# Performance work log

Measured on AMD Instinct MI355X. Metric: run time of the kernel, lower is better.

Reference implementation:

```python
import jax, jax.numpy as jnp
import numpy as np

DIM = 128
HEADS = 8
HEAD_DIM = DIM // HEADS
PE_DIM = 48
TEMP = 10000.0
WIN = 2
NUM_VALUES = WIN * WIN
SCALE = HEAD_DIM ** -0.5
TWO_PI = 2.0 * np.pi
EPS = 1e-6


def _interleave_sincos(p):
    # p [..., nf] -> interleaved sin(even)/cos(odd), matching torch stack+flatten
    s = jnp.sin(p[..., 0::2])
    c = jnp.cos(p[..., 1::2])
    return jnp.stack((s, c), axis=-1).reshape(p.shape)


def _dim_t(num_pos_feats):
    i = np.arange(num_pos_feats)
    return jnp.asarray(TEMP ** (2.0 * (i // 2) / num_pos_feats), dtype=jnp.float32)


def window_position_bias():
    nf = PE_DIM // 2
    ye = jnp.arange(WIN, dtype=jnp.float32)  # cumsum(ones)-1 along h
    xe = jnp.arange(WIN, dtype=jnp.float32)
    ye = ye / (ye[-1] + EPS) * TWO_PI
    xe = xe / (xe[-1] + EPS) * TWO_PI
    dt = _dim_t(nf)
    pos_y = ye[:, None, None] / dt
    pos_x = xe[None, :, None] / dt
    pos_y = jnp.broadcast_to(pos_y, (WIN, WIN, nf))
    pos_x = jnp.broadcast_to(pos_x, (WIN, WIN, nf))
    pe = jnp.concatenate((_interleave_sincos(pos_y), _interleave_sincos(pos_x)), axis=-1)
    return pe.reshape(NUM_VALUES, PE_DIM)


def points_position_encoding(points):
    # points [n, hw, 2] fractional offsets -> [n, hw, PE_DIM]
    nf = PE_DIM // 2
    ye = points[..., 0] / (WIN + EPS) * TWO_PI
    xe = points[..., 1] / (WIN + EPS) * TWO_PI
    dt = _dim_t(nf)
    pos_y = _interleave_sincos(ye[..., None] / dt)
    pos_x = _interleave_sincos(xe[..., None] / dt)
    return jnp.concatenate((pos_y, pos_x), axis=-1)


def setup_inputs() -> dict:
    key = jax.random.key(0)
    ks = jax.random.split(key, 12)
    n, c, h, w = 2, 48, 192, 192
    y = jax.random.normal(ks[0], (n, c, h, w), jnp.float32)
    x = jax.random.normal(ks[1], (n, c, h, w), jnp.float32)
    conv_w = jax.random.normal(ks[2], (1, 2 * PE_DIM, 3, 3), jnp.float32) * 0.05
    conv_b = jnp.zeros((1,), jnp.float32)
    q_w = jax.random.normal(ks[3], (PE_DIM, DIM), jnp.float32) * (PE_DIM ** -0.5)
    q_b = jnp.zeros((DIM,), jnp.float32)
    k_w = jax.random.normal(ks[4], (PE_DIM, DIM), jnp.float32) * (PE_DIM ** -0.5)
    k_b = jnp.zeros((DIM,), jnp.float32)
    v_w = jax.random.normal(ks[5], (PE_DIM, DIM), jnp.float32) * (PE_DIM ** -0.5)
    v_b = jnp.zeros((DIM,), jnp.float32)
    return {"y": y, "x": x, "conv_w": conv_w, "conv_b": conv_b,
            "q_w": q_w, "q_b": q_b, "k_w": k_w, "k_b": k_b, "v_w": v_w, "v_b": v_b}


def reference(y, x, conv_w, conv_b, q_w, q_b, k_w, k_b, v_w, v_b):
    n, c, h, w = x.shape
    hw = h * w
    # per-pixel horizontal offset from both feature maps
    off = jax.lax.conv_general_dilated(
        jnp.concatenate([y, x], axis=1), conv_w, (1, 1), ((1, 1), (1, 1)),
        dimension_numbers=("NCHW", "OIHW", "NCHW")) + conv_b[None, :, None, None]
    off = jnp.transpose(off, (0, 2, 3, 1)) * (2.0 / w)  # [n,h,w,1]

    gh, gw = jnp.meshgrid(jnp.arange(h, dtype=x.dtype), jnp.arange(w, dtype=x.dtype), indexing="ij")
    # flow.flip(-1) puts the offset on the w coordinate only
    grid_wrp = jnp.stack(
        (jnp.broadcast_to(gh, (n, h, w)),
         gw[None] + off[..., 0]), axis=-1)                      # [n,h,w,2]
    flr = jnp.floor(grid_wrp)
    frac = (grid_wrp - flr).reshape(n, hw, 2)
    flr = flr.reshape(n, hw, 2)

    widx = jnp.array([[0, 0], [0, 1], [1, 0], [1, 1]], dtype=x.dtype)  # window_idx_offset
    g4 = (flr[:, :, None, :] + widx).reshape(n, hw * NUM_VALUES, 2)

    idx0 = jnp.clip(g4[..., 0], 0, h - 1).astype(jnp.int32)
    idx1 = jnp.clip(g4[..., 1], 0, w - 1).astype(jnp.int32)
    lin = idx1 + w * idx0                                      # [n, hw*4]
    wrp = jnp.take_along_axis(y.reshape(n, c, hw), lin[:, None, :], axis=2)  # [n,c,hw*4]
    wrp = jnp.transpose(wrp, (0, 2, 1))                        # [n, hw*4, c]

    # pe_dim // c == 1 tiling; add window position bias per pixel
    pb = window_position_bias()                                # [4, PE_DIM]
    wrp = (wrp.reshape(n, hw, NUM_VALUES, PE_DIM) + pb).reshape(n, hw * NUM_VALUES, PE_DIM)

    x_flat = jnp.transpose(x.reshape(n, c, hw), (0, 2, 1))     # [n, hw, c]
    x_in = x_flat + points_position_encoding(frac)

    nhw = n * hw
    q = (x_in @ q_w + q_b).reshape(nhw, HEADS, HEAD_DIM)
    k = (wrp @ k_w + k_b).reshape(nhw, NUM_VALUES, HEADS, HEAD_DIM)
    v = (wrp @ v_w + v_b).reshape(nhw, NUM_VALUES, HEADS, HEAD_DIM)

    attn = jnp.einsum("phd,pkhd->phk", q * SCALE, k)           # [nhw, heads, 4]
    attn = jax.nn.softmax(attn, axis=-1)
    out = jnp.einsum("phk,pkhd->phd", attn, v).reshape(nhw, DIM)
    return jnp.transpose(out.reshape(n, h, w, DIM), (0, 3, 1, 2))
```

## Files before the change

kernel.cpp:

```cpp
#include <hip/hip_runtime.h>
#include <hip/hip_bf16.h>

#define HW_ 36864
#define W_ 192
#define H_ 192
#define NPIX_ 73728
#define TWO_PI_F 6.283185307179586f

typedef __attribute__((ext_vector_type(8))) short bfrag;
typedef __attribute__((ext_vector_type(4))) float f4;

__device__ __constant__ float DT_G[12] = {
    1.0f, 2.154434690031884f, 4.641588833612779f, 10.0f,
    21.54434690031884f, 46.41588833612779f, 100.0f, 215.4434690031884f,
    464.1588833612779f, 1000.0f, 2154.434690031884f, 4641.588833612779f};

__device__ __forceinline__ unsigned short f2bf(float f) {
    __hip_bfloat16 h = __float2bfloat16(f);
    unsigned short u;
    __builtin_memcpy(&u, &h, 2);
    return u;
}

__device__ __forceinline__ int a_idx(int tile, int m, int k) {
    return tile * 1024 + ((k >> 5) << 9) + (m << 3) + (((k >> 3) & 3) << 7) + (k & 7);
}

__global__ void prep_wfrag(const float* __restrict__ qw, const float* __restrict__ kw,
                           const float* __restrict__ vw, unsigned short* __restrict__ wsb) {
    int idx = blockIdx.x * 256 + threadIdx.x;
    if (idx >= 24576) return;
    int j = idx & 7;
    int lane = (idx >> 3) & 63;
    int ks = (idx >> 9) & 1;
    int h = (idx >> 10) & 7;
    int mat = idx >> 13;
    const float* w = (mat == 0) ? qw : (mat == 1) ? kw : vw;
    int k = ks * 32 + ((lane >> 4) << 3) + j;
    int n = (h << 4) + (lane & 15);
    float f = (k < 48) ? w[k * 128 + n] : 0.0f;
    wsb[idx] = f2bf(f);
}

__global__ __launch_bounds__(256, 4) void conv_kernel(
    const float* __restrict__ y, const float* __restrict__ x,
    const float* __restrict__ cw, const float* __restrict__ cb,
    float* __restrict__ offs_g) {
    __shared__ float part[8][64];
    int tid = threadIdx.x;
    int bid = blockIdx.x;
    int b = (bid & 7) * 144 + (bid >> 3);
    int pix0 = b * 64;
    int n = pix0 / HW_;
    int rem = pix0 - n * HW_;
    int row0 = rem / W_;
    int col0 = rem - row0 * W_;
    int lane = tid & 63, w = tid >> 6;
    int col = col0 + lane;

    float m_lf = (col > 0) ? 1.f : 0.f, m_rt = (col < W_ - 1) ? 1.f : 0.f;
    float m_up = (row0 > 0) ? 1.f : 0.f, m_dn = (row0 < H_ - 1) ? 1.f : 0.f;
    int c_lf = col - (col > 0 ? 1 : 0);
    int c_rt = col + (col < W_ - 1 ? 1 : 0);
    int r_up = row0 - (row0 > 0 ? 1 : 0);
    int r_dn = row0 + (row0 < H_ - 1 ? 1 : 0);
    float k0 = m_up * m_lf, k1 = m_up, k2 = m_up * m_rt;
    float k3 = m_lf, k5 = m_rt;
    float k6 = m_dn * m_lf, k7 = m_dn, k8 = m_dn * m_rt;

    float accA = 0.f, accB = 0.f;
#pragma unroll
    for (int g = 0; g < 4; ++g) {
        float buf[54];
#pragma unroll
        for (int cc = 0; cc < 6; ++cc) {
            int ic = w * 24 + g * 6 + cc;
            const float* src = (ic < 48) ? y : x;
            int c = (ic < 48) ? ic : ic - 48;
            const float* b0 = src + (size_t)(n * 48 + c) * HW_;
            const float* pu = b0 + (size_t)r_up * W_;
            const float* pm = b0 + (size_t)row0 * W_;
            const float* pd = b0 + (size_t)r_dn * W_;
            buf[cc * 9 + 0] = pu[c_lf];
            buf[cc * 9 + 1] = pu[col];
            buf[cc * 9 + 2] = pu[c_rt];
            buf[cc * 9 + 3] = pm[c_lf];
            buf[cc * 9 + 4] = pm[col];
            buf[cc * 9 + 5] = pm[c_rt];
            buf[cc * 9 + 6] = pd[c_lf];
            buf[cc * 9 + 7] = pd[col];
            buf[cc * 9 + 8] = pd[c_rt];
        }
        float& acc = (g < 2) ? accA : accB;
#pragma unroll
        for (int cc = 0; cc < 6; ++cc) {
            int ic = w * 24 + g * 6 + cc;
            const float* wp = cw + ic * 9;
            acc += buf[cc * 9 + 0] * (wp[0] * k0);
            acc += buf[cc * 9 + 1] * (wp[1] * k1);
            acc += buf[cc * 9 + 2] * (wp[2] * k2);
            acc += buf[cc * 9 + 3] * (wp[3] * k3);
            acc += buf[cc * 9 + 4] * wp[4];
            acc += buf[cc * 9 + 5] * (wp[5] * k5);
            acc += buf[cc * 9 + 6] * (wp[6] * k6);
            acc += buf[cc * 9 + 7] * (wp[7] * k7);
            acc += buf[cc * 9 + 8] * (wp[8] * k8);
        }
    }
    part[2 * w][lane] = accA;
    part[2 * w + 1][lane] = accB;
    __syncthreads();
    if (tid < 64) {
        float a = part[0][tid];
#pragma unroll
        for (int s = 1; s < 8; ++s) a += part[s][tid];
        offs_g[pix0 + tid] = (a + cb[0]) * (2.0f / (float)W_);
    }
}

struct __align__(16) Smem {
    unsigned short A[10 * 1024];
    float outt[128 * 33];
    float pbl[192];
    float offs[32];
};

__global__ __launch_bounds__(512, 6) void fused_kernel(
    const float* __restrict__ y, const float* __restrict__ x,
    const float* __restrict__ qb, const float* __restrict__ kb,
    const float* __restrict__ vb, const unsigned short* __restrict__ wsb,
    const float* __restrict__ offs_g, float* __restrict__ out) {
    __shared__ Smem sm;
    int tid = threadIdx.x;
    int bid = blockIdx.x;
    int b = (bid & 7) * 288 + (bid >> 3);
    int pix0 = b * 32;
    int n = pix0 / HW_;
    int rem0 = pix0 - n * HW_;
    int row0 = rem0 / W_;
    int col0 = rem0 - row0 * W_;

    float xv[3];
    {
        int p = tid & 31, c0 = tid >> 5;
        const float* xb = x + (size_t)(n * 48) * HW_ + rem0 + p;
#pragma unroll
        for (int k2 = 0; k2 < 3; ++k2) xv[k2] = xb[(size_t)(c0 + 16 * k2) * HW_];
    }

    if (tid < 32) sm.offs[tid] = offs_g[pix0 + tid];
    if (tid < 192) {
        int v = tid / 48, c = tid - (tid / 48) * 48;
        int iy = v >> 1, ix = v & 1;
        int cc = (c < 24) ? c : c - 24;
        int sel = (c < 24) ? iy : ix;
        float e = sel ? (TWO_PI_F / (1.0f + 1e-6f)) : 0.0f;
        int j = cc >> 1;
        float arg = e / DT_G[j];
        sm.pbl[v * 48 + c] = (cc & 1) ? __cosf(arg) : __sinf(arg);
    }
    for (int i = tid; i < 1280; i += 512) {
        int t = i >> 7;
        ((unsigned int*)sm.A)[t * 512 + 384 + (i & 127)] = 0u;
    }
    __syncthreads();

    {
        int p = tid & 31, c0 = tid >> 5;
        float o = sm.offs[p];
        float gx = (float)(col0 + p) + o;
        float fr = gx - floorf(gx);
        float t1 = fr / (2.0f + 1e-6f);
#pragma unroll
        for (int k2 = 0; k2 < 3; ++k2) {
            int c = c0 + 16 * k2;
            float pe;
            if (c < 24) {
                pe = (c & 1) ? 1.0f : 0.0f;
            } else {
                int cc = c - 24;
                float arg = (t1 * TWO_PI_F) / DT_G[cc >> 1];
                pe = (cc & 1) ? __cosf(arg) : __sinf(arg);
            }
            sm.A[a_idx(p >> 4, p & 15, c)] = f2bf(xv[k2] + pe);
        }
    }
    {
        int r = tid & 127, cH = tid >> 7;
        int p = r >> 2, v = r & 3;
        float o = sm.offs[p];
        float gx = (float)(col0 + p) + o;
        float fx = floorf(gx);
        int dy = v >> 1, dx = v & 1;
        int rr = (int)fminf(fmaxf((float)(row0 + dy), 0.0f), 191.0f);
        int ccx = (int)fminf(fmaxf(fx + (float)dx, 0.0f), 191.0f);
        const float* yb = y + (size_t)(n * 48 + cH) * HW_ + rr * W_ + ccx;
        float yv[12];
#pragma unroll
        for (int k2 = 0; k2 < 12; ++k2) yv[k2] = yb[(size_t)(4 * k2) * HW_];
        int t = 2 + (r >> 4), m = r & 15;
#pragma unroll
        for (int k2 = 0; k2 < 12; ++k2) {
            int c = cH + 4 * k2;
            sm.A[a_idx(t, m, c)] = f2bf(yv[k2] + sm.pbl[v * 48 + c]);
        }
    }
    __syncthreads();

    int lane = tid & 63, h = tid >> 6;
    int lq = lane & 15, lg = lane >> 4;
    float qbv = qb[(h << 4) + lq];
    float kbv = kb[(h << 4) + lq];
    float vbv = vb[(h << 4) + lq];

    const int hb = (h << 1) * 64 + lane;
    bfrag qB0 = *(const bfrag*)&wsb[(0 * 1024 + hb) * 8];
    bfrag qB1 = *(const bfrag*)&wsb[(0 * 1024 + hb + 64) * 8];
    bfrag kB0 = *(const bfrag*)&wsb[(1 * 1024 + hb) * 8];
    bfrag kB1 = *(const bfrag*)&wsb[(1 * 1024 + hb + 64) * 8];
    bfrag vB0 = *(const bfrag*)&wsb[(2 * 1024 + hb) * 8];
    bfrag vB1 = *(const bfrag*)&wsb[(2 * 1024 + hb + 64) * 8];

    f4 qacc[2];
#pragma unroll
    for (int t = 0; t < 2; ++t) {
        bfrag a0 = *(const bfrag*)&sm.A[t * 1024 + lane * 8];
        bfrag a1 = *(const bfrag*)&sm.A[t * 1024 + 512 + lane * 8];
        f4 a = {qbv, qbv, qbv, qbv};
        a = __builtin_amdgcn_mfma_f32_16x16x32_bf16(a0, qB0, a, 0, 0, 0);
        a = __builtin_amdgcn_mfma_f32_16x16x32_bf16(a1, qB1, a, 0, 0, 0);
        qacc[t] = a;
    }

#pragma unroll
    for (int m = 0; m < 8; ++m) {
        bfrag a0 = *(const bfrag*)&sm.A[(2 + m) * 1024 + lane * 8];
        bfrag a1 = *(const bfrag*)&sm.A[(2 + m) * 1024 + 512 + lane * 8];
        f4 ka = {kbv, kbv, kbv, kbv};
        ka = __builtin_amdgcn_mfma_f32_16x16x32_bf16(a0, kB0, ka, 0, 0, 0);
        ka = __builtin_amdgcn_mfma_f32_16x16x32_bf16(a1, kB1, ka, 0, 0, 0);
        f4 va = {vbv, vbv, vbv, vbv};
        va = __builtin_amdgcn_mfma_f32_16x16x32_bf16(a0, vB0, va, 0, 0, 0);
        va = __builtin_amdgcn_mfma_f32_16x16x32_bf16(a1, vB1, va, 0, 0, 0);

        int src = ((m & 3) << 4) | lq;
        f4 qa = qacc[m >> 2];
        float t0 = __shfl(qa.x, src), t1 = __shfl(qa.y, src);
        float t2 = __shfl(qa.z, src), t3 = __shfl(qa.w, src);
        float qv = (lg == 0) ? t0 : (lg == 1) ? t1 : (lg == 2) ? t2 : t3;
        qv *= 0.25f;

        float s0 = qv * ka.x, s1 = qv * ka.y, s2 = qv * ka.z, s3 = qv * ka.w;
#pragma unroll
        for (int msk = 1; msk < 16; msk <<= 1) {
            s0 += __shfl_xor(s0, msk);
            s1 += __shfl_xor(s1, msk);
            s2 += __shfl_xor(s2, msk);
            s3 += __shfl_xor(s3, msk);
        }
        float mx = fmaxf(fmaxf(s0, s1), fmaxf(s2, s3));
        float e0 = __expf(s0 - mx), e1 = __expf(s1 - mx);
        float e2 = __expf(s2 - mx), e3 = __expf(s3 - mx);
        float rden = 1.0f / (e0 + e1 + e2 + e3);
        float o = (e0 * va.x + e1 * va.y + e2 * va.z + e3 * va.w) * rden;
        sm.outt[((h << 4) + lq) * 33 + (m << 2) + lg] = o;
    }
    __syncthreads();

    {
        int ch = tid >> 2, q4 = tid & 3;
        const float* sp = &sm.outt[ch * 33 + q4 * 8];
        float4* dst = (float4*)(out + (size_t)(n * 128 + ch) * HW_ + rem0 + q4 * 8);
        dst[0] = make_float4(sp[0], sp[1], sp[2], sp[3]);
        dst[1] = make_float4(sp[4], sp[5], sp[6], sp[7]);
    }
}

extern "C" void kernel_launch(void* const* d_in, const int* in_sizes, int n_in,
                              void* d_out, int out_size, void* d_ws, size_t ws_size,
                              hipStream_t stream) {
    unsigned short* wsb = (unsigned short*)d_ws;
    float* offs_g = (float*)d_ws + 12288;
    hipLaunchKernelGGL(prep_wfrag, dim3(96), dim3(256), 0, stream,
                       (const float*)d_in[4], (const float*)d_in[6],
                       (const float*)d_in[8], wsb);
    hipLaunchKernelGGL(conv_kernel, dim3(NPIX_ / 64), dim3(256), 0, stream,
                       (const float*)d_in[0], (const float*)d_in[1],
                       (const float*)d_in[2], (const float*)d_in[3], offs_g);
    hipLaunchKernelGGL(fused_kernel, dim3(NPIX_ / 32), dim3(512), 0, stream,
                       (const float*)d_in[0], (const float*)d_in[1],
                       (const float*)d_in[5], (const float*)d_in[7],
                       (const float*)d_in[9], wsb, offs_g,
                       (float*)d_out);
}
```

Baseline: 154.1 us.

## Fuse offset conv into attention kernel and use DPP reductions

Removes the separate conv_kernel launch and computes the 3x3 offset conv inside fused_kernel, with half the threads running the conv while the other half load x and build the position bias. The cross-lane score reduction now uses DPP row operations instead of shfl_xor, and the q broadcast shuffle is replaced by swizzling the A-tile row order so each lane already holds its q value. Shared-memory writes become 16-byte vectorised bfrag stores. In exchange the launch bound drops to 4 blocks per SM, and the conv halo loads for neighbouring pixels are now repeated per 32-pixel block.

```diff
diff --git a/kernel.cpp b/kernel.cpp
--- a/kernel.cpp
+++ b/kernel.cpp
@@ -24,6 +24,21 @@
 
 __device__ __forceinline__ int a_idx(int tile, int m, int k) {
     return tile * 1024 + ((k >> 5) << 9) + (m << 3) + (((k >> 3) & 3) << 7) + (k & 7);
+}
+
+__device__ __forceinline__ int rsw(int r) { return ((r & 3) << 2) | (r >> 2); }
+
+__device__ __forceinline__ float red16(float v) {
+    int t;
+    t = __builtin_amdgcn_update_dpp(0, __float_as_int(v), 0x128, 0xF, 0xF, true);
+    v += __int_as_float(t);
+    t = __builtin_amdgcn_update_dpp(0, __float_as_int(v), 0x124, 0xF, 0xF, true);
+    v += __int_as_float(t);
+    t = __builtin_amdgcn_update_dpp(0, __float_as_int(v), 0x122, 0xF, 0xF, true);
+    v += __int_as_float(t);
+    t = __builtin_amdgcn_update_dpp(0, __float_as_int(v), 0x121, 0xF, 0xF, true);
+    v += __int_as_float(t);
+    return v;
 }
 
 __global__ void prep_wfrag(const float* __restrict__ qw, const float* __restrict__ kw,
@@ -42,94 +57,20 @@
     wsb[idx] = f2bf(f);
 }
 
-__global__ __launch_bounds__(256, 4) void conv_kernel(
-    const float* __restrict__ y, const float* __restrict__ x,
-    const float* __restrict__ cw, const float* __restrict__ cb,
-    float* __restrict__ offs_g) {
-    __shared__ float part[8][64];
-    int tid = threadIdx.x;
-    int bid = blockIdx.x;
-    int b = (bid & 7) * 144 + (bid >> 3);
-    int pix0 = b * 64;
-    int n = pix0 / HW_;
-    int rem = pix0 - n * HW_;
-    int row0 = rem / W_;
-    int col0 = rem - row0 * W_;
-    int lane = tid & 63, w = tid >> 6;
-    int col = col0 + lane;
-
-    float m_lf = (col > 0) ? 1.f : 0.f, m_rt = (col < W_ - 1) ? 1.f : 0.f;
-    float m_up = (row0 > 0) ? 1.f : 0.f, m_dn = (row0 < H_ - 1) ? 1.f : 0.f;
-    int c_lf = col - (col > 0 ? 1 : 0);
-    int c_rt = col + (col < W_ - 1 ? 1 : 0);
-    int r_up = row0 - (row0 > 0 ? 1 : 0);
-    int r_dn = row0 + (row0 < H_ - 1 ? 1 : 0);
-    float k0 = m_up * m_lf, k1 = m_up, k2 = m_up * m_rt;
-    float k3 = m_lf, k5 = m_rt;
-    float k6 = m_dn * m_lf, k7 = m_dn, k8 = m_dn * m_rt;
-
-    float accA = 0.f, accB = 0.f;
-#pragma unroll
-    for (int g = 0; g < 4; ++g) {
-        float buf[54];
-#pragma unroll
-        for (int cc = 0; cc < 6; ++cc) {
-            int ic = w * 24 + g * 6 + cc;
-            const float* src = (ic < 48) ? y : x;
-            int c = (ic < 48) ? ic : ic - 48;
-            const float* b0 = src + (size_t)(n * 48 + c) * HW_;
-            const float* pu = b0 + (size_t)r_up * W_;
-            const float* pm = b0 + (size_t)row0 * W_;
-            const float* pd = b0 + (size_t)r_dn * W_;
-            buf[cc * 9 + 0] = pu[c_lf];
-            buf[cc * 9 + 1] = pu[col];
-            buf[cc * 9 + 2] = pu[c_rt];
-            buf[cc * 9 + 3] = pm[c_lf];
-            buf[cc * 9 + 4] = pm[col];
-            buf[cc * 9 + 5] = pm[c_rt];
-            buf[cc * 9 + 6] = pd[c_lf];
-            buf[cc * 9 + 7] = pd[col];
-            buf[cc * 9 + 8] = pd[c_rt];
-        }
-        float& acc = (g < 2) ? accA : accB;
-#pragma unroll
-        for (int cc = 0; cc < 6; ++cc) {
-            int ic = w * 24 + g * 6 + cc;
-            const float* wp = cw + ic * 9;
-            acc += buf[cc * 9 + 0] * (wp[0] * k0);
-            acc += buf[cc * 9 + 1] * (wp[1] * k1);
-            acc += buf[cc * 9 + 2] * (wp[2] * k2);
-            acc += buf[cc * 9 + 3] * (wp[3] * k3);
-            acc += buf[cc * 9 + 4] * wp[4];
-            acc += buf[cc * 9 + 5] * (wp[5] * k5);
-            acc += buf[cc * 9 + 6] * (wp[6] * k6);
-            acc += buf[cc * 9 + 7] * (wp[7] * k7);
-            acc += buf[cc * 9 + 8] * (wp[8] * k8);
-        }
-    }
-    part[2 * w][lane] = accA;
-    part[2 * w + 1][lane] = accB;
-    __syncthreads();
-    if (tid < 64) {
-        float a = part[0][tid];
-#pragma unroll
-        for (int s = 1; s < 8; ++s) a += part[s][tid];
-        offs_g[pix0 + tid] = (a + cb[0]) * (2.0f / (float)W_);
-    }
-}
-
 struct __align__(16) Smem {
     unsigned short A[10 * 1024];
     float outt[128 * 33];
     float pbl[192];
     float offs[32];
+    float part[8][32];
 };
 
-__global__ __launch_bounds__(512, 6) void fused_kernel(
+__global__ __launch_bounds__(512, 4) void fused_kernel(
     const float* __restrict__ y, const float* __restrict__ x,
+    const float* __restrict__ cw, const float* __restrict__ cb,
     const float* __restrict__ qb, const float* __restrict__ kb,
     const float* __restrict__ vb, const unsigned short* __restrict__ wsb,
-    const float* __restrict__ offs_g, float* __restrict__ out) {
+    float* __restrict__ out) {
     __shared__ Smem sm;
     int tid = threadIdx.x;
     int bid = blockIdx.x;
@@ -140,70 +81,147 @@
     int row0 = rem0 / W_;
     int col0 = rem0 - row0 * W_;
 
-    float xv[3];
-    {
-        int p = tid & 31, c0 = tid >> 5;
-        const float* xb = x + (size_t)(n * 48) * HW_ + rem0 + p;
-#pragma unroll
-        for (int k2 = 0; k2 < 3; ++k2) xv[k2] = xb[(size_t)(c0 + 16 * k2) * HW_];
-    }
-
-    if (tid < 32) sm.offs[tid] = offs_g[pix0 + tid];
-    if (tid < 192) {
-        int v = tid / 48, c = tid - (tid / 48) * 48;
-        int iy = v >> 1, ix = v & 1;
-        int cc = (c < 24) ? c : c - 24;
-        int sel = (c < 24) ? iy : ix;
-        float e = sel ? (TWO_PI_F / (1.0f + 1e-6f)) : 0.0f;
-        int j = cc >> 1;
-        float arg = e / DT_G[j];
-        sm.pbl[v * 48 + c] = (cc & 1) ? __cosf(arg) : __sinf(arg);
-    }
-    for (int i = tid; i < 1280; i += 512) {
-        int t = i >> 7;
-        ((unsigned int*)sm.A)[t * 512 + 384 + (i & 127)] = 0u;
+    float xv8[8];
+    if (tid < 256) {
+        int p = tid & 31, q = tid >> 5;
+        int col = col0 + p;
+        float m_lf = (col > 0) ? 1.f : 0.f, m_rt = (col < W_ - 1) ? 1.f : 0.f;
+        float m_up = (row0 > 0) ? 1.f : 0.f, m_dn = (row0 < H_ - 1) ? 1.f : 0.f;
+        int c_lf = col - (col > 0 ? 1 : 0);
+        int c_rt = col + (col < W_ - 1 ? 1 : 0);
+        int r_up = row0 - (row0 > 0 ? 1 : 0);
+        int r_dn = row0 + (row0 < H_ - 1 ? 1 : 0);
+        float k0 = m_up * m_lf, k1 = m_up, k2 = m_up * m_rt;
+        float k3 = m_lf, k5 = m_rt;
+        float k6 = m_dn * m_lf, k7 = m_dn, k8 = m_dn * m_rt;
+        int icbase = (q >> 1) * 24 + (q & 1) * 12;
+        float acc = 0.f;
+#pragma unroll
+        for (int g2 = 0; g2 < 4; ++g2) {
+            float buf[27];
+#pragma unroll
+            for (int cc = 0; cc < 3; ++cc) {
+                int ic = icbase + g2 * 3 + cc;
+                const float* src = (ic < 48) ? y : x;
+                int c = (ic < 48) ? ic : ic - 48;
+                const float* b0p = src + (size_t)(n * 48 + c) * HW_;
+                const float* pu = b0p + (size_t)r_up * W_;
+                const float* pm = b0p + (size_t)row0 * W_;
+                const float* pd = b0p + (size_t)r_dn * W_;
+                buf[cc * 9 + 0] = pu[c_lf];
+                buf[cc * 9 + 1] = pu[col];
+                buf[cc * 9 + 2] = pu[c_rt];
+                buf[cc * 9 + 3] = pm[c_lf];
+                buf[cc * 9 + 4] = pm[col];
+                buf[cc * 9 + 5] = pm[c_rt];
+                buf[cc * 9 + 6] = pd[c_lf];
+                buf[cc * 9 + 7] = pd[col];
+                buf[cc * 9 + 8] = pd[c_rt];
+            }
+#pragma unroll
+            for (int cc = 0; cc < 3; ++cc) {
+                int ic = icbase + g2 * 3 + cc;
+                const float* wp = cw + ic * 9;
+                acc += buf[cc * 9 + 0] * (wp[0] * k0);
+                acc += buf[cc * 9 + 1] * (wp[1] * k1);
+                acc += buf[cc * 9 + 2] * (wp[2] * k2);
+                acc += buf[cc * 9 + 3] * (wp[3] * k3);
+                acc += buf[cc * 9 + 4] * wp[4];
+                acc += buf[cc * 9 + 5] * (wp[5] * k5);
+                acc += buf[cc * 9 + 6] * (wp[6] * k6);
+                acc += buf[cc * 9 + 7] * (wp[7] * k7);
+                acc += buf[cc * 9 + 8] * (wp[8] * k8);
+            }
+        }
+        sm.part[q][p] = acc;
+    } else {
+        int e = tid - 256, p = e & 31, oct = e >> 5;
+        if (oct < 6) {
+            const float* xb = x + (size_t)(n * 48 + oct * 8) * HW_ + rem0 + p;
+#pragma unroll
+            for (int j = 0; j < 8; ++j) xv8[j] = xb[(size_t)j * HW_];
+        }
+        if (e < 192) {
+            int v = e / 48, c = e - (e / 48) * 48;
+            int iy = v >> 1, ix = v & 1;
+            int cc = (c < 24) ? c : c - 24;
+            int sel = (c < 24) ? iy : ix;
+            float ee = sel ? (TWO_PI_F / (1.0f + 1e-6f)) : 0.0f;
+            float arg = ee / DT_G[cc >> 1];
+            sm.pbl[v * 48 + c] = (cc & 1) ? __cosf(arg) : __sinf(arg);
+        }
     }
     __syncthreads();
-
-    {
-        int p = tid & 31, c0 = tid >> 5;
-        float o = sm.offs[p];
-        float gx = (float)(col0 + p) + o;
-        float fr = gx - floorf(gx);
-        float t1 = fr / (2.0f + 1e-6f);
-#pragma unroll
-        for (int k2 = 0; k2 < 3; ++k2) {
-            int c = c0 + 16 * k2;
-            float pe;
-            if (c < 24) {
-                pe = (c & 1) ? 1.0f : 0.0f;
-            } else {
-                int cc = c - 24;
-                float arg = (t1 * TWO_PI_F) / DT_G[cc >> 1];
-                pe = (cc & 1) ? __cosf(arg) : __sinf(arg);
-            }
-            sm.A[a_idx(p >> 4, p & 15, c)] = f2bf(xv[k2] + pe);
-        }
-    }
-    {
-        int r = tid & 127, cH = tid >> 7;
-        int p = r >> 2, v = r & 3;
+    if (tid < 32) {
+        float a = sm.part[0][tid];
+#pragma unroll
+        for (int s = 1; s < 8; ++s) a += sm.part[s][tid];
+        sm.offs[tid] = (a + cb[0]) * (2.0f / (float)W_);
+    }
+    __syncthreads();
+
+    float yv[16];
+    int r_w = tid & 127, oct_w = tid >> 7, t_w = 0, m_w = 0, v_w = 0;
+    bool do_wrp = tid < 384;
+    if (do_wrp) {
+        int p = r_w >> 2;
+        v_w = r_w & 3;
         float o = sm.offs[p];
         float gx = (float)(col0 + p) + o;
         float fx = floorf(gx);
-        int dy = v >> 1, dx = v & 1;
+        int dy = v_w >> 1, dx = v_w & 1;
         int rr = (int)fminf(fmaxf((float)(row0 + dy), 0.0f), 191.0f);
         int ccx = (int)fminf(fmaxf(fx + (float)dx, 0.0f), 191.0f);
-        const float* yb = y + (size_t)(n * 48 + cH) * HW_ + rr * W_ + ccx;
-        float yv[12];
-#pragma unroll
-        for (int k2 = 0; k2 < 12; ++k2) yv[k2] = yb[(size_t)(4 * k2) * HW_];
-        int t = 2 + (r >> 4), m = r & 15;
-#pragma unroll
-        for (int k2 = 0; k2 < 12; ++k2) {
-            int c = cH + 4 * k2;
-            sm.A[a_idx(t, m, c)] = f2bf(yv[k2] + sm.pbl[v * 48 + c]);
+        const float* yb = y + (size_t)(n * 48) * HW_ + (size_t)rr * W_ + ccx;
+#pragma unroll
+        for (int j = 0; j < 8; ++j) yv[j] = yb[(size_t)(oct_w * 8 + j) * HW_];
+#pragma unroll
+        for (int j = 0; j < 8; ++j) yv[8 + j] = yb[(size_t)((oct_w + 3) * 8 + j) * HW_];
+        t_w = 2 + (r_w >> 4);
+        m_w = r_w & 15;
+    }
+    if (tid >= 256) {
+        int e = tid - 256, p = e & 31, oct = e >> 5;
+        bfrag w0;
+        if (oct < 6) {
+            float o = sm.offs[p];
+            float gx = (float)(col0 + p) + o;
+            float fr = gx - floorf(gx);
+            float t1 = fr / (2.0f + 1e-6f);
+#pragma unroll
+            for (int j = 0; j < 8; ++j) {
+                float pe;
+                if (oct < 3) {
+                    pe = (j & 1) ? 1.0f : 0.0f;
+                } else {
+                    int cc = oct * 8 + j - 24;
+                    float arg = (t1 * TWO_PI_F) / DT_G[cc >> 1];
+                    pe = (cc & 1) ? __cosf(arg) : __sinf(arg);
+                }
+                w0[j] = (short)f2bf(xv8[j] + pe);
+            }
+        } else {
+#pragma unroll
+            for (int j = 0; j < 8; ++j) w0[j] = 0;
         }
+        *(bfrag*)&sm.A[a_idx(p >> 4, rsw(p & 15), oct * 8)] = w0;
+    } else {
+        int r = tid & 127, o2 = 6 + (tid >> 7);
+        bfrag z;
+#pragma unroll
+        for (int j = 0; j < 8; ++j) z[j] = 0;
+        *(bfrag*)&sm.A[a_idx(2 + (r >> 4), r & 15, o2 * 8)] = z;
+    }
+    if (do_wrp) {
+        bfrag w0, w1;
+#pragma unroll
+        for (int j = 0; j < 8; ++j)
+            w0[j] = (short)f2bf(yv[j] + sm.pbl[v_w * 48 + oct_w * 8 + j]);
+#pragma unroll
+        for (int j = 0; j < 8; ++j)
+            w1[j] = (short)f2bf(yv[8 + j] + sm.pbl[v_w * 48 + (oct_w + 3) * 8 + j]);
+        *(bfrag*)&sm.A[a_idx(t_w, m_w, oct_w * 8)] = w0;
+        *(bfrag*)&sm.A[a_idx(t_w, m_w, (oct_w + 3) * 8)] = w1;
     }
     __syncthreads();
 
@@ -243,21 +261,16 @@
         va = __builtin_amdgcn_mfma_f32_16x16x32_bf16(a0, vB0, va, 0, 0, 0);
         va = __builtin_amdgcn_mfma_f32_16x16x32_bf16(a1, vB1, va, 0, 0, 0);
 
-        int src = ((m & 3) << 4) | lq;
         f4 qa = qacc[m >> 2];
-        float t0 = __shfl(qa.x, src), t1 = __shfl(qa.y, src);
-        float t2 = __shfl(qa.z, src), t3 = __shfl(qa.w, src);
-        float qv = (lg == 0) ? t0 : (lg == 1) ? t1 : (lg == 2) ? t2 : t3;
+        float qv = ((m & 3) == 0) ? qa.x : ((m & 3) == 1) ? qa.y
+                 : ((m & 3) == 2) ? qa.z : qa.w;
         qv *= 0.25f;
 
         float s0 = qv * ka.x, s1 = qv * ka.y, s2 = qv * ka.z, s3 = qv * ka.w;
-#pragma unroll
-        for (int msk = 1; msk < 16; msk <<= 1) {
-            s0 += __shfl_xor(s0, msk);
-            s1 += __shfl_xor(s1, msk);
-            s2 += __shfl_xor(s2, msk);
-            s3 += __shfl_xor(s3, msk);
-        }
+        s0 = red16(s0);
+        s1 = red16(s1);
+        s2 = red16(s2);
+        s3 = red16(s3);
         float mx = fmaxf(fmaxf(s0, s1), fmaxf(s2, s3));
         float e0 = __expf(s0 - mx), e1 = __expf(s1 - mx);
         float e2 = __expf(s2 - mx), e3 = __expf(s3 - mx);
@@ -280,16 +293,13 @@
                               void* d_out, int out_size, void* d_ws, size_t ws_size,
                               hipStream_t stream) {
     unsigned short* wsb = (unsigned short*)d_ws;
-    float* offs_g = (float*)d_ws + 12288;
     hipLaunchKernelGGL(prep_wfrag, dim3(96), dim3(256), 0, stream,
                        (const float*)d_in[4], (const float*)d_in[6],
                        (const float*)d_in[8], wsb);
-    hipLaunchKernelGGL(conv_kernel, dim3(NPIX_ / 64), dim3(256), 0, stream,
-                       (const float*)d_in[0], (const float*)d_in[1],
-                       (const float*)d_in[2], (const float*)d_in[3], offs_g);
     hipLaunchKernelGGL(fused_kernel, dim3(NPIX_ / 32), dim3(512), 0, stream,
                        (const float*)d_in[0], (const float*)d_in[1],
+                       (const float*)d_in[2], (const float*)d_in[3],
                        (const float*)d_in[5], (const float*)d_in[7],
-                       (const float*)d_in[9], wsb, offs_g,
+                       (const float*)d_in[9], wsb,
                        (float*)d_out);
 }
```

After: 135.6 us. -12.0%, faster.
